# Optimization experiments

Hardware: AMD Instinct MI355X
Metric: run time of the kernel (lower is better)

The kernel has to match this reference:

```python
import jax, jax.numpy as jnp
import numpy as np

B, R, C, D = 4, 64, 64, 512   # batch, rows, cols, hidden_size
H, DH = 4, 128                # num_heads, channels per head
S = R * C                     # flattened attention length (raster order)
NEG = -1e6                    # mask value used by coltran


def setup_inputs():
    key = jax.random.key(0)
    ks = jax.random.split(key, 7)
    def w(k, shape, s=0.02):
        return jax.random.normal(k, shape, jnp.float32) * s
    return dict(
        x=jax.random.normal(ks[0], (B, R, C, D), jnp.float32),
        wq=w(ks[1], (D, H, DH)),
        wk=w(ks[2], (D, H, DH)),
        wv=w(ks[3], (D, H, DH)),
        wo=w(ks[4], (H, DH, D)),
        # relative_attention_bias_i: [num_heads, 2*length] per axis
        # (zero-init in the original; randomized here so the bias path is exercised)
        rel_row=w(ks[5], (H, 2 * R)),
        rel_col=w(ks[6], (H, 2 * C)),
    )


def _axis_bias(w, L):
    """att_utils.relative_attn_bias: [H, 2L] -> [H, Lq, Lk], b[h,q,k] = w[h, L-1 + k - q]."""
    pos = jnp.arange(L)
    idx = (L - 1) + pos[None, :] - pos[:, None]  # [Lq, Lk] in [0, 2L-2]
    return w[:, idx]


def reference(x, wq, wk, wv, wo, rel_row, rel_col):
    # q/k/v projections: contract channel axis into [H, DH]
    q = jnp.einsum('brcd,dhe->brche', x, wq) * (DH ** -0.5)
    k = jnp.einsum('brcd,dhe->brche', x, wk)
    v = jnp.einsum('brcd,dhe->brche', x, wv)
    q = q.reshape(B, S, H, DH)
    k = k.reshape(B, S, H, DH)
    v = v.reshape(B, S, H, DH)

    # factorized N-D relative attention bias -> [H, S, S]
    brow = _axis_bias(rel_row, R)  # [H, R, R]
    bcol = _axis_bias(rel_col, C)  # [H, C, C]
    bias = (brow[:, :, None, :, None] + bcol[:, None, :, None, :]).reshape(H, S, S)

    # 'future' mask in raster order: disallow k > q
    mask = jnp.triu(jnp.full((S, S), NEG, dtype=jnp.float32), 1)

    logits = jnp.einsum('bqhe,bkhe->bhqk', q, k) + bias[None] + mask[None, None]
    p = jax.nn.softmax(logits, axis=-1)
    o = jnp.einsum('bhqk,bkhe->bqhe', p, v)       # weighted sum over keys
    out = jnp.einsum('bqhe,hed->bqd', o, wo)      # final projection, contract_axes=2
    return out.reshape(B, R, C, D)
```

## Files before the change

### kernel.cpp

```cpp
#include <hip/hip_runtime.h>
#include <cstdint>

typedef unsigned short u16;
typedef __attribute__((ext_vector_type(8))) short short8;
typedef __attribute__((ext_vector_type(4))) short short4v;
typedef __attribute__((ext_vector_type(4))) float f32x4;
typedef __attribute__((ext_vector_type(4))) unsigned short u16x4;
typedef __attribute__((ext_vector_type(2))) float f32x2;
typedef __attribute__((ext_vector_type(2))) __bf16 bf16x2;


#if defined(__has_builtin)
#if __has_builtin(__builtin_amdgcn_mfma_f32_16x16x16bf16_1k)
#define HAVE_MFMA16 1
#endif
#endif

__device__ __forceinline__ uint32_t pk2(float a, float b) {
  f32x2 t;
  t[0] = a;
  t[1] = b;
  bf16x2 h = __builtin_convertvector(t, bf16x2);
  return __builtin_bit_cast(uint32_t, h);
}

__device__ __forceinline__ u16 f2b(float f) {
  return __builtin_bit_cast(u16, (__bf16)f);
}

__device__ __forceinline__ uint2 pkbf16x4(f32x4 v, float s) {
  uint2 r;
  r.x = pk2(v[0] * s, v[1] * s);
  r.y = pk2(v[2] * s, v[3] * s);
  return r;
}

__device__ __forceinline__ void dma16(const u16* g, u16* l) {
  __builtin_amdgcn_global_load_lds(
      (const __attribute__((address_space(1))) unsigned int*)(uintptr_t)g,
      (__attribute__((address_space(3))) unsigned int*)(uintptr_t)l, 16, 0, 0);
}

#define LDS_FENCE() asm volatile("s_waitcnt lgkmcnt(0)" ::: "memory")

__global__ __launch_bounds__(256) void xcast(const float* __restrict__ x,
                                             u16* __restrict__ xb) {
  const size_t i = (size_t)(blockIdx.x * 256 + threadIdx.x) * 8;
  const float4 a = *(const float4*)(x + i);
  const float4 b = *(const float4*)(x + i + 4);
  uint4 o;
  o.x = pk2(a.x, a.y);
  o.y = pk2(a.z, a.w);
  o.z = pk2(b.x, b.y);
  o.w = pk2(b.z, b.w);
  *(uint4*)(xb + i) = o;
}

__global__ __launch_bounds__(256) void transpose_all(const float* __restrict__ wq,
                                                     const float* __restrict__ wk,
                                                     const float* __restrict__ wv,
                                                     const float* __restrict__ wo,
                                                     u16* __restrict__ wT,
                                                     u16* __restrict__ woT) {
  __shared__ __align__(16) u16 T[64][68];
  const int mtx = blockIdx.y;
  const float* src = (mtx == 0) ? wq : (mtx == 1) ? wk : (mtx == 2) ? wv : wo;
  u16* dst = (mtx < 3) ? (wT + (size_t)mtx * 262144) : woT;
  const int tr = blockIdx.x >> 3, tc = blockIdx.x & 7;
  const int tid = threadIdx.x;
#pragma unroll
  for (int p = 0; p < 4; ++p) {
    int i = p * 256 + tid;
    int row = i >> 4, c4 = i & 15;
    float4 v = *(const float4*)(src + (size_t)(tr * 64 + row) * 512 + tc * 64 + c4 * 4);
    T[c4 * 4 + 0][row] = f2b(v.x);
    T[c4 * 4 + 1][row] = f2b(v.y);
    T[c4 * 4 + 2][row] = f2b(v.z);
    T[c4 * 4 + 3][row] = f2b(v.w);
  }
  __syncthreads();
#pragma unroll
  for (int p = 0; p < 4; ++p) {
    int i = p * 256 + tid;
    int row = i >> 4, c4 = i & 15;
    *(u16x4*)(dst + (size_t)(tc * 64 + row) * 512 + tr * 64 + c4 * 4) =
        *(const u16x4*)&T[row][c4 * 4];
  }
}

__global__ __launch_bounds__(512, 2) void qkv_gemm(const u16* __restrict__ xb,
                                                   const u16* __restrict__ wT_all,
                                                   u16* __restrict__ qbuf,
                                                   u16* __restrict__ kbuf,
                                                   u16* __restrict__ vtbuf) {
  __shared__ __align__(16) u16 smem[128 * 72 + 256 * 72];
  u16* As = smem;
  u16* Bs = smem + 128 * 72;
  const int tid = threadIdx.x;
  const int wave = tid >> 6, lane = tid & 63, quad = lane >> 4, l16 = lane & 15;
  const int wm = wave >> 2, wn = wave & 3;
  const int m0 = blockIdx.x * 128;
  const int which = blockIdx.y >> 1;
  const int n0 = (blockIdx.y & 1) * 256;
  const u16* wTb = wT_all + (size_t)which * 262144 + (size_t)n0 * 512;

  f32x4 acc[4][4];
  const f32x4 fz = {0.f, 0.f, 0.f, 0.f};
#pragma unroll
  for (int i = 0; i < 4; ++i)
#pragma unroll
    for (int j = 0; j < 4; ++j) acc[i][j] = fz;

  for (int k0 = 0; k0 < 512; k0 += 64) {
#pragma unroll
    for (int p = 0; p < 2; ++p) {
      int i = p * 512 + tid, row = i >> 3, c8 = i & 7;
      uint4 v = *(const uint4*)(xb + (size_t)(m0 + row) * 512 + k0 + c8 * 8);
      *(uint4*)&As[row * 72 + c8 * 8] = v;
    }
#pragma unroll
    for (int p = 0; p < 4; ++p) {
      int i = p * 512 + tid, row = i >> 3, c8 = i & 7;
      uint4 v = *(const uint4*)(wTb + (size_t)row * 512 + k0 + c8 * 8);
      *(uint4*)&Bs[row * 72 + c8 * 8] = v;
    }
    __syncthreads();
#pragma unroll
    for (int ks = 0; ks < 2; ++ks) {
      short8 xf[4], wf[4];
#pragma unroll
      for (int mt = 0; mt < 4; ++mt)
        xf[mt] = *(const short8*)&As[(wm * 64 + mt * 16 + l16) * 72 + ks * 32 + quad * 8];
#pragma unroll
      for (int nt = 0; nt < 4; ++nt)
        wf[nt] = *(const short8*)&Bs[(wn * 64 + nt * 16 + l16) * 72 + ks * 32 + quad * 8];
      if (which < 2) {
#pragma unroll
        for (int mt = 0; mt < 4; ++mt)
#pragma unroll
          for (int nt = 0; nt < 4; ++nt)
            acc[mt][nt] = __builtin_amdgcn_mfma_f32_16x16x32_bf16(wf[nt], xf[mt],
                                                                  acc[mt][nt], 0, 0, 0);
      } else {
#pragma unroll
        for (int mt = 0; mt < 4; ++mt)
#pragma unroll
          for (int nt = 0; nt < 4; ++nt)
            acc[mt][nt] = __builtin_amdgcn_mfma_f32_16x16x32_bf16(xf[mt], wf[nt],
                                                                  acc[mt][nt], 0, 0, 0);
      }
    }
    __syncthreads();
  }
  u16* sw = smem + wave * 3072;
  const int dhg0 = n0 + wn * 64;
  const int h = dhg0 >> 7, dhh0 = dhg0 & 127;
  const int bq = m0 >> 12;
  const int bh = bq * 4 + h;
  const int sl0 = (m0 & 4095) + wm * 64;

  if (which < 2) {
    const float scl = (which == 0) ? 0.08838834764831845f : 1.0f;
    u16* dst = (which == 0) ? qbuf : kbuf;
#pragma unroll
    for (int mt = 0; mt < 4; ++mt) {
      LDS_FENCE();
#pragma unroll
      for (int nt = 0; nt < 4; ++nt)
        *(uint2*)&sw[l16 * 68 + nt * 16 + quad * 4] = pkbf16x4(acc[mt][nt], scl);
      LDS_FENCE();
#pragma unroll
      for (int p = 0; p < 2; ++p) {
        const int sr = p * 8 + (lane >> 3), dl = (lane & 7) * 8;
        uint4 v = *(const uint4*)&sw[sr * 68 + dl];
        const int sl = sl0 + mt * 16 + sr;
        *(uint4*)(dst + ((size_t)(bh * 4096 + sl)) * 128 + dhh0 + dl) = v;
      }
    }
  } else {
#pragma unroll
    for (int p2 = 0; p2 < 2; ++p2) {
      LDS_FENCE();
#pragma unroll
      for (int m2 = 0; m2 < 2; ++m2) {
        const int mt = p2 * 2 + m2;
#pragma unroll
        for (int nt = 0; nt < 4; ++nt)
          *(uint2*)&sw[(nt * 16 + l16) * 36 + m2 * 16 + quad * 4] =
              pkbf16x4(acc[mt][nt], 1.0f);
      }
      LDS_FENCE();
#pragma unroll
      for (int j = 0; j < 4; ++j) {
        const int dl = j * 16 + (lane >> 2), so = (lane & 3) * 8;
        uint4 v = *(const uint4*)&sw[dl * 36 + so];
        const int sl = sl0 + p2 * 32 + so;
        *(uint4*)(vtbuf + ((size_t)(bh * 128 + dhh0 + dl)) * 4096 + sl) = v;
      }
    }
  }
}

__global__ __launch_bounds__(256, 4) void attn(const u16* __restrict__ qbuf,
                                               const u16* __restrict__ kbuf,
                                               const u16* __restrict__ vtbuf,
                                               const float* __restrict__ rel_row,
                                               const float* __restrict__ rel_col,
                                               u16* __restrict__ obuf) {
  __shared__ __align__(16) u16 KsF[64 * 128];
  __shared__ __align__(16) u16 VtF[128 * 64];
#ifndef HAVE_MFMA16
  __shared__ __align__(16) u16 Plds[4][16][72];
#endif
  __shared__ float rcol[128];
  __shared__ float rrow[128];

  const int tid = threadIdx.x;
  const int wave = tid >> 6, lane = tid & 63, quad = lane >> 4, l16 = lane & 15;
  const int g = blockIdx.x & 255, jq = blockIdx.x >> 8;
  const int t = g >> 4, bh = g & 15;
  const int qt = (jq == 0) ? (63 - t) : (jq == 1) ? t : (jq == 2) ? (47 - t) : (16 + t);
  const int b = bh >> 2, h = bh & 3;

  const float LOG2E = 1.4426950408889634f;
  if (tid < 128) rcol[tid] = rel_col[h * 128 + tid] * LOG2E;
  else rrow[tid - 128] = rel_row[h * 128 + (tid - 128)] * LOG2E;

  const int q_loc = wave * 16 + l16;
  const int q_glob = qt * 64 + q_loc;
  const int qc = q_loc;

  const u16* qrow = qbuf + ((size_t)bh * 4096 + q_glob) * 128;
  short8 qf[4];
#pragma unroll
  for (int ks = 0; ks < 4; ++ks) qf[ks] = *(const short8*)(qrow + ks * 32 + quad * 8);

  __syncthreads();

  float rc2[4][4];
#pragma unroll
  for (int nt = 0; nt < 4; ++nt)
#pragma unroll
    for (int r = 0; r < 4; ++r)
      rc2[nt][r] = rcol[63 + nt * 16 + quad * 4 + r - qc];

  const f32x4 fz = {0.f, 0.f, 0.f, 0.f};
  f32x4 oacc[8];
#pragma unroll
  for (int i = 0; i < 8; ++i) oacc[i] = fz;
  float l_run = 0.0f;

  const u16* kbase = kbuf + (size_t)bh * 4096 * 128;
  const u16* vbase = vtbuf + (size_t)bh * 128 * 4096;
  const int krow = tid >> 4, kcs = ((tid & 15) ^ (krow & 7)) * 8;
  const int vrow = tid >> 3, vcs = ((tid & 7) ^ (vrow & 7)) * 8;
  u16* kdst = KsF + wave * 512;
  u16* vdst = VtF + wave * 512;

  for (int kt = 0; kt <= qt; ++kt) {
    __syncthreads();
    {
      const u16* ksrc = kbase + (size_t)kt * 8192;
      const u16* vsrc = vbase + kt * 64;
#pragma unroll
      for (int j = 0; j < 4; ++j)
        dma16(ksrc + (size_t)(j * 16 + krow) * 128 + kcs, kdst + j * 2048);
#pragma unroll
      for (int j = 0; j < 4; ++j)
        dma16(vsrc + (size_t)(j * 32 + vrow) * 4096 + vcs, vdst + j * 2048);
    }
    __syncthreads();

    f32x4 sacc[4];
#pragma unroll
    for (int nt = 0; nt < 4; ++nt) sacc[nt] = fz;
    __builtin_amdgcn_s_setprio(1);
#pragma unroll
    for (int ks = 0; ks < 4; ++ks)
#pragma unroll
      for (int nt = 0; nt < 4; ++nt) {
        short8 kf = *(const short8*)&KsF[(nt * 16 + l16) * 128 +
                                         ((ks * 32 + quad * 8) ^ ((l16 & 7) * 8))];
        sacc[nt] = __builtin_amdgcn_mfma_f32_16x16x32_bf16(kf, qf[ks], sacc[nt], 0, 0, 0);
      }
    __builtin_amdgcn_s_setprio(0);

    const float browl = rrow[63 + kt - qt];
    const bool diag = (kt == qt);
    uint2 pd[4];
#pragma unroll
    for (int nt = 0; nt < 4; ++nt) {
      f32x4 pv;
#pragma unroll
      for (int r = 0; r < 4; ++r) {
        const int kc2 = nt * 16 + quad * 4 + r;
        float p = __builtin_amdgcn_exp2f(fmaf(sacc[nt][r], LOG2E, rc2[nt][r] + browl));
        if (diag && kc2 > qc) p = 0.0f;
        l_run += p;
        pv[r] = p;
      }
      pd[nt].x = pk2(pv[0], pv[1]);
      pd[nt].y = pk2(pv[2], pv[3]);
    }

#ifdef HAVE_MFMA16
    __builtin_amdgcn_s_setprio(1);
#pragma unroll
    for (int nt = 0; nt < 4; ++nt) {
      short4v pf = __builtin_bit_cast(short4v, pd[nt]);
#pragma unroll
      for (int mt = 0; mt < 8; ++mt) {
        short4v vf = *(const short4v*)&VtF[(mt * 16 + l16) * 64 +
                                           ((nt * 16 + quad * 4) ^ ((l16 & 7) * 8))];
        oacc[mt] = __builtin_amdgcn_mfma_f32_16x16x16bf16_1k(vf, pf, oacc[mt], 0, 0, 0);
      }
    }
    __builtin_amdgcn_s_setprio(0);
#else
#pragma unroll
    for (int nt = 0; nt < 4; ++nt)
      *(uint2*)&Plds[wave][l16][nt * 16 + quad * 4] = pd[nt];
#pragma unroll
    for (int ks2 = 0; ks2 < 2; ++ks2) {
      short8 pf = *(const short8*)&Plds[wave][l16][ks2 * 32 + quad * 8];
#pragma unroll
      for (int mt = 0; mt < 8; ++mt) {
        short8 vf = *(const short8*)&VtF[(mt * 16 + l16) * 64 +
                                         ((ks2 * 32 + quad * 8) ^ ((l16 & 7) * 8))];
        oacc[mt] = __builtin_amdgcn_mfma_f32_16x16x32_bf16(vf, pf, oacc[mt], 0, 0, 0);
      }
    }
#endif
  }

  l_run += __shfl_xor(l_run, 16);
  l_run += __shfl_xor(l_run, 32);
  const float inv_l = 1.0f / l_run;
  u16* orow = obuf + ((size_t)b * 4096 + q_glob) * 512 + h * 128;
#pragma unroll
  for (int mt = 0; mt < 8; ++mt)
    *(uint2*)(orow + mt * 16 + quad * 4) = pkbf16x4(oacc[mt], inv_l);
}

__global__ __launch_bounds__(512, 2) void out_gemm(const u16* __restrict__ obuf,
                                                   const u16* __restrict__ woT,
                                                   float* __restrict__ out) {
  __shared__ __align__(16) u16 smem[128 * 72 + 256 * 72];
  u16* As = smem;
  u16* Bs = smem + 128 * 72;
  const int tid = threadIdx.x;
  const int wave = tid >> 6, lane = tid & 63, quad = lane >> 4, l16 = lane & 15;
  const int wm = wave >> 2, wn = wave & 3;
  const int m0 = blockIdx.x * 128;
  const int n0 = blockIdx.y * 256;

  f32x4 acc[4][4];
  const f32x4 fz = {0.f, 0.f, 0.f, 0.f};
#pragma unroll
  for (int i = 0; i < 4; ++i)
#pragma unroll
    for (int j = 0; j < 4; ++j) acc[i][j] = fz;

  for (int k0 = 0; k0 < 512; k0 += 64) {
#pragma unroll
    for (int p = 0; p < 2; ++p) {
      int i = p * 512 + tid, row = i >> 3, c8 = i & 7;
      uint4 v = *(const uint4*)(obuf + (size_t)(m0 + row) * 512 + k0 + c8 * 8);
      *(uint4*)&As[row * 72 + c8 * 8] = v;
    }
#pragma unroll
    for (int p = 0; p < 4; ++p) {
      int i = p * 512 + tid, row = i >> 3, c8 = i & 7;
      uint4 v = *(const uint4*)(woT + (size_t)(n0 + row) * 512 + k0 + c8 * 8);
      *(uint4*)&Bs[row * 72 + c8 * 8] = v;
    }
    __syncthreads();
#pragma unroll
    for (int ks = 0; ks < 2; ++ks) {
      short8 of[4], wf[4];
#pragma unroll
      for (int mt = 0; mt < 4; ++mt)
        of[mt] = *(const short8*)&As[(wm * 64 + mt * 16 + l16) * 72 + ks * 32 + quad * 8];
#pragma unroll
      for (int nt = 0; nt < 4; ++nt)
        wf[nt] = *(const short8*)&Bs[(wn * 64 + nt * 16 + l16) * 72 + ks * 32 + quad * 8];
#pragma unroll
      for (int mt = 0; mt < 4; ++mt)
#pragma unroll
        for (int nt = 0; nt < 4; ++nt)
          acc[mt][nt] = __builtin_amdgcn_mfma_f32_16x16x32_bf16(wf[nt], of[mt],
                                                                acc[mt][nt], 0, 0, 0);
    }
    __syncthreads();
  }

  float* swf = (float*)smem + wave * 1536;
#pragma unroll
  for (int mt = 0; mt < 4; ++mt) {
    LDS_FENCE();
#pragma unroll
    for (int nt = 0; nt < 4; ++nt)
      *(f32x4*)&swf[l16 * 68 + nt * 16 + quad * 4] = acc[mt][nt];
    LDS_FENCE();
#pragma unroll
    for (int p = 0; p < 4; ++p) {
      const int sr = p * 4 + (lane >> 4), dl = l16 * 4;
      float4 v = *(const float4*)&swf[sr * 68 + dl];
      const int s = m0 + wm * 64 + mt * 16 + sr;
      *(float4*)(out + (size_t)s * 512 + n0 + wn * 64 + dl) = v;
    }
  }
}

extern "C" void kernel_launch(void* const* d_in, const int* in_sizes, int n_in,
                              void* d_out, int out_size, void* d_ws, size_t ws_size,
                              hipStream_t stream) {
  const float* x       = (const float*)d_in[0];
  const float* wq      = (const float*)d_in[1];
  const float* wk      = (const float*)d_in[2];
  const float* wv      = (const float*)d_in[3];
  const float* wo      = (const float*)d_in[4];
  const float* rel_row = (const float*)d_in[5];
  const float* rel_col = (const float*)d_in[6];
  float* out = (float*)d_out;

  char* ws = (char*)d_ws;
  u16* wT    = (u16*)(ws);
  u16* woT   = (u16*)(ws + 1572864);
  u16* qbuf  = (u16*)(ws + 2097152);
  u16* kbuf  = (u16*)(ws + 2097152 + 16777216);
  u16* vtbuf = (u16*)(ws + 2097152 + 2 * 16777216);
  u16* obuf  = (u16*)(ws + 2097152 + 3 * 16777216);
  u16* xb    = obuf;

  xcast<<<4096, 256, 0, stream>>>(x, xb);
  transpose_all<<<dim3(64, 4), 256, 0, stream>>>(wq, wk, wv, wo, wT, woT);
  qkv_gemm<<<dim3(128, 6), 512, 0, stream>>>(xb, wT, qbuf, kbuf, vtbuf);
  attn<<<1024, 256, 0, stream>>>(qbuf, kbuf, vtbuf, rel_row, rel_col, obuf);
  out_gemm<<<dim3(128, 2), 512, 0, stream>>>(obuf, woT, out);
}
```

Measured before the change: 298.6 us.

## Prefetch next K/V tile into registers instead of direct LDS DMA

Replaces global_load_lds DMA with register-staged loads of the next K/V tile, issued after the LDS write so global latency overlaps compute. It also switches the XOR-swizzled LDS layout to padded rows and simplifies block-to-tile mapping to descending qt order. The cost is extra VGPRs and LDS, which may lower occupancy, and the loss of the balanced causal-work interleave.

```diff
diff --git a/kernel.cpp b/kernel.cpp
--- a/kernel.cpp
+++ b/kernel.cpp
@@ -33,12 +33,6 @@
   r.x = pk2(v[0] * s, v[1] * s);
   r.y = pk2(v[2] * s, v[3] * s);
   return r;
-}
-
-__device__ __forceinline__ void dma16(const u16* g, u16* l) {
-  __builtin_amdgcn_global_load_lds(
-      (const __attribute__((address_space(1))) unsigned int*)(uintptr_t)g,
-      (__attribute__((address_space(3))) unsigned int*)(uintptr_t)l, 16, 0, 0);
 }
 
 #define LDS_FENCE() asm volatile("s_waitcnt lgkmcnt(0)" ::: "memory")
@@ -207,8 +201,8 @@
                                                const float* __restrict__ rel_row,
                                                const float* __restrict__ rel_col,
                                                u16* __restrict__ obuf) {
-  __shared__ __align__(16) u16 KsF[64 * 128];
-  __shared__ __align__(16) u16 VtF[128 * 64];
+  __shared__ __align__(16) u16 Ks[64][136];
+  __shared__ __align__(16) u16 Vt[128][72];
 #ifndef HAVE_MFMA16
   __shared__ __align__(16) u16 Plds[4][16][72];
 #endif
@@ -217,9 +211,8 @@
 
   const int tid = threadIdx.x;
   const int wave = tid >> 6, lane = tid & 63, quad = lane >> 4, l16 = lane & 15;
-  const int g = blockIdx.x & 255, jq = blockIdx.x >> 8;
-  const int t = g >> 4, bh = g & 15;
-  const int qt = (jq == 0) ? (63 - t) : (jq == 1) ? t : (jq == 2) ? (47 - t) : (16 + t);
+  const int bh = blockIdx.x & 15;
+  const int qt = 63 - (blockIdx.x >> 4);
   const int b = bh >> 2, h = bh & 3;
 
   const float LOG2E = 1.4426950408889634f;
@@ -252,24 +245,34 @@
 
   const u16* kbase = kbuf + (size_t)bh * 4096 * 128;
   const u16* vbase = vtbuf + (size_t)bh * 128 * 4096;
-  const int krow = tid >> 4, kcs = ((tid & 15) ^ (krow & 7)) * 8;
-  const int vrow = tid >> 3, vcs = ((tid & 7) ^ (vrow & 7)) * 8;
-  u16* kdst = KsF + wave * 512;
-  u16* vdst = VtF + wave * 512;
+  const int kr = tid >> 4, kc = (tid & 15) * 8;
+  const int vr = tid >> 3, vc = (tid & 7) * 8;
+
+  uint4 kreg[4], vreg[4];
+#pragma unroll
+  for (int j = 0; j < 4; ++j)
+    kreg[j] = *(const uint4*)(kbase + (size_t)(j * 16 + kr) * 128 + kc);
+#pragma unroll
+  for (int j = 0; j < 4; ++j)
+    vreg[j] = *(const uint4*)(vbase + (size_t)(j * 32 + vr) * 4096 + vc);
 
   for (int kt = 0; kt <= qt; ++kt) {
     __syncthreads();
-    {
-      const u16* ksrc = kbase + (size_t)kt * 8192;
-      const u16* vsrc = vbase + kt * 64;
+#pragma unroll
+    for (int j = 0; j < 4; ++j) *(uint4*)&Ks[j * 16 + kr][kc] = kreg[j];
+#pragma unroll
+    for (int j = 0; j < 4; ++j) *(uint4*)&Vt[j * 32 + vr][vc] = vreg[j];
+    __syncthreads();
+    if (kt < qt) {
+      const u16* ksrc = kbase + (size_t)(kt + 1) * 8192;
+      const u16* vsrc = vbase + (kt + 1) * 64;
 #pragma unroll
       for (int j = 0; j < 4; ++j)
-        dma16(ksrc + (size_t)(j * 16 + krow) * 128 + kcs, kdst + j * 2048);
+        kreg[j] = *(const uint4*)(ksrc + (size_t)(j * 16 + kr) * 128 + kc);
 #pragma unroll
       for (int j = 0; j < 4; ++j)
-        dma16(vsrc + (size_t)(j * 32 + vrow) * 4096 + vcs, vdst + j * 2048);
-    }
-    __syncthreads();
+        vreg[j] = *(const uint4*)(vsrc + (size_t)(j * 32 + vr) * 4096 + vc);
+    }
 
     f32x4 sacc[4];
 #pragma unroll
@@ -279,8 +282,7 @@
     for (int ks = 0; ks < 4; ++ks)
 #pragma unroll
       for (int nt = 0; nt < 4; ++nt) {
-        short8 kf = *(const short8*)&KsF[(nt * 16 + l16) * 128 +
-                                         ((ks * 32 + quad * 8) ^ ((l16 & 7) * 8))];
+        short8 kf = *(const short8*)&Ks[nt * 16 + l16][ks * 32 + quad * 8];
         sacc[nt] = __builtin_amdgcn_mfma_f32_16x16x32_bf16(kf, qf[ks], sacc[nt], 0, 0, 0);
       }
     __builtin_amdgcn_s_setprio(0);
@@ -310,8 +312,7 @@
       short4v pf = __builtin_bit_cast(short4v, pd[nt]);
 #pragma unroll
       for (int mt = 0; mt < 8; ++mt) {
-        short4v vf = *(const short4v*)&VtF[(mt * 16 + l16) * 64 +
-                                           ((nt * 16 + quad * 4) ^ ((l16 & 7) * 8))];
+        short4v vf = *(const short4v*)&Vt[mt * 16 + l16][nt * 16 + quad * 4];
         oacc[mt] = __builtin_amdgcn_mfma_f32_16x16x16bf16_1k(vf, pf, oacc[mt], 0, 0, 0);
       }
     }
@@ -325,8 +326,7 @@
       short8 pf = *(const short8*)&Plds[wave][l16][ks2 * 32 + quad * 8];
 #pragma unroll
       for (int mt = 0; mt < 8; ++mt) {
-        short8 vf = *(const short8*)&VtF[(mt * 16 + l16) * 64 +
-                                         ((ks2 * 32 + quad * 8) ^ ((l16 & 7) * 8))];
+        short8 vf = *(const short8*)&Vt[mt * 16 + l16][ks2 * 32 + quad * 8];
         oacc[mt] = __builtin_amdgcn_mfma_f32_16x16x32_bf16(vf, pf, oacc[mt], 0, 0, 0);
       }
     }
```

Measured after the change: 508.9 us. 1.7x slower.

## Balance causal attention work by pairing rows and splitting long rows across blocks

Applied to the files above, without the earlier changes.

The causal attention grid changes from one query tile per block to balanced work units. Each half-0 block handles one short row plus the first half of a long row, and each half-1 block handles the second half of that long row. The partial outputs and softmax denominators go to fp32 workspace, and a new onorm kernel combines and normalizes them. This gives every block the same number of key tiles, removing tail imbalance, at the cost of extra fp32 partial traffic and an additional kernel launch.

```diff
diff --git a/kernel.cpp b/kernel.cpp
--- a/kernel.cpp
+++ b/kernel.cpp
@@ -206,7 +206,9 @@
                                                const u16* __restrict__ vtbuf,
                                                const float* __restrict__ rel_row,
                                                const float* __restrict__ rel_col,
-                                               u16* __restrict__ obuf) {
+                                               u16* __restrict__ obuf,
+                                               float* __restrict__ opart,
+                                               float* __restrict__ lpart) {
   __shared__ __align__(16) u16 KsF[64 * 128];
   __shared__ __align__(16) u16 VtF[128 * 64];
 #ifndef HAVE_MFMA16
@@ -217,9 +219,8 @@
 
   const int tid = threadIdx.x;
   const int wave = tid >> 6, lane = tid & 63, quad = lane >> 4, l16 = lane & 15;
-  const int g = blockIdx.x & 255, jq = blockIdx.x >> 8;
-  const int t = g >> 4, bh = g & 15;
-  const int qt = (jq == 0) ? (63 - t) : (jq == 1) ? t : (jq == 2) ? (47 - t) : (16 + t);
+  const int jid = blockIdx.x;
+  const int bh = jid & 15, p = (jid >> 4) & 31, half = jid >> 9;
   const int b = bh >> 2, h = bh & 3;
 
   const float LOG2E = 1.4426950408889634f;
@@ -227,13 +228,7 @@
   else rrow[tid - 128] = rel_row[h * 128 + (tid - 128)] * LOG2E;
 
   const int q_loc = wave * 16 + l16;
-  const int q_glob = qt * 64 + q_loc;
   const int qc = q_loc;
-
-  const u16* qrow = qbuf + ((size_t)bh * 4096 + q_glob) * 128;
-  short8 qf[4];
-#pragma unroll
-  for (int ks = 0; ks < 4; ++ks) qf[ks] = *(const short8*)(qrow + ks * 32 + quad * 8);
 
   __syncthreads();
 
@@ -245,11 +240,6 @@
       rc2[nt][r] = rcol[63 + nt * 16 + quad * 4 + r - qc];
 
   const f32x4 fz = {0.f, 0.f, 0.f, 0.f};
-  f32x4 oacc[8];
-#pragma unroll
-  for (int i = 0; i < 8; ++i) oacc[i] = fz;
-  float l_run = 0.0f;
-
   const u16* kbase = kbuf + (size_t)bh * 4096 * 128;
   const u16* vbase = vtbuf + (size_t)bh * 128 * 4096;
   const int krow = tid >> 4, kcs = ((tid & 15) ^ (krow & 7)) * 8;
@@ -257,89 +247,141 @@
   u16* kdst = KsF + wave * 512;
   u16* vdst = VtF + wave * 512;
 
-  for (int kt = 0; kt <= qt; ++kt) {
-    __syncthreads();
-    {
-      const u16* ksrc = kbase + (size_t)kt * 8192;
-      const u16* vsrc = vbase + kt * 64;
-#pragma unroll
-      for (int j = 0; j < 4; ++j)
-        dma16(ksrc + (size_t)(j * 16 + krow) * 128 + kcs, kdst + j * 2048);
-#pragma unroll
-      for (int j = 0; j < 4; ++j)
-        dma16(vsrc + (size_t)(j * 32 + vrow) * 4096 + vcs, vdst + j * 2048);
-    }
-    __syncthreads();
-
-    f32x4 sacc[4];
-#pragma unroll
-    for (int nt = 0; nt < 4; ++nt) sacc[nt] = fz;
-    __builtin_amdgcn_s_setprio(1);
-#pragma unroll
-    for (int ks = 0; ks < 4; ++ks)
+  auto run_row = [&](int r, int ktb, int kte, bool direct) {
+    const u16* qrow = qbuf + ((size_t)bh * 4096 + r * 64 + q_loc) * 128;
+    short8 qf[4];
+#pragma unroll
+    for (int ks = 0; ks < 4; ++ks) qf[ks] = *(const short8*)(qrow + ks * 32 + quad * 8);
+    f32x4 oacc[8];
+#pragma unroll
+    for (int i = 0; i < 8; ++i) oacc[i] = fz;
+    float l_run = 0.0f;
+
+    for (int kt = ktb; kt < kte; ++kt) {
+      __syncthreads();
+      {
+        const u16* ksrc = kbase + (size_t)kt * 8192;
+        const u16* vsrc = vbase + kt * 64;
+#pragma unroll
+        for (int j = 0; j < 4; ++j)
+          dma16(ksrc + (size_t)(j * 16 + krow) * 128 + kcs, kdst + j * 2048);
+#pragma unroll
+        for (int j = 0; j < 4; ++j)
+          dma16(vsrc + (size_t)(j * 32 + vrow) * 4096 + vcs, vdst + j * 2048);
+      }
+      __syncthreads();
+
+      f32x4 sacc[4];
+#pragma unroll
+      for (int nt = 0; nt < 4; ++nt) sacc[nt] = fz;
+      __builtin_amdgcn_s_setprio(1);
+#pragma unroll
+      for (int ks = 0; ks < 4; ++ks)
+#pragma unroll
+        for (int nt = 0; nt < 4; ++nt) {
+          short8 kf = *(const short8*)&KsF[(nt * 16 + l16) * 128 +
+                                           ((ks * 32 + quad * 8) ^ ((l16 & 7) * 8))];
+          sacc[nt] = __builtin_amdgcn_mfma_f32_16x16x32_bf16(kf, qf[ks], sacc[nt], 0, 0, 0);
+        }
+      __builtin_amdgcn_s_setprio(0);
+
+      const float browl = rrow[63 + kt - r];
+      const bool diag = (kt == r);
+      uint2 pd[4];
 #pragma unroll
       for (int nt = 0; nt < 4; ++nt) {
-        short8 kf = *(const short8*)&KsF[(nt * 16 + l16) * 128 +
-                                         ((ks * 32 + quad * 8) ^ ((l16 & 7) * 8))];
-        sacc[nt] = __builtin_amdgcn_mfma_f32_16x16x32_bf16(kf, qf[ks], sacc[nt], 0, 0, 0);
-      }
-    __builtin_amdgcn_s_setprio(0);
-
-    const float browl = rrow[63 + kt - qt];
-    const bool diag = (kt == qt);
-    uint2 pd[4];
-#pragma unroll
-    for (int nt = 0; nt < 4; ++nt) {
-      f32x4 pv;
-#pragma unroll
-      for (int r = 0; r < 4; ++r) {
-        const int kc2 = nt * 16 + quad * 4 + r;
-        float p = __builtin_amdgcn_exp2f(fmaf(sacc[nt][r], LOG2E, rc2[nt][r] + browl));
-        if (diag && kc2 > qc) p = 0.0f;
-        l_run += p;
-        pv[r] = p;
-      }
-      pd[nt].x = pk2(pv[0], pv[1]);
-      pd[nt].y = pk2(pv[2], pv[3]);
-    }
+        f32x4 pv;
+#pragma unroll
+        for (int rr = 0; rr < 4; ++rr) {
+          const int kc2 = nt * 16 + quad * 4 + rr;
+          float pe = __builtin_amdgcn_exp2f(fmaf(sacc[nt][rr], LOG2E, rc2[nt][rr] + browl));
+          if (diag && kc2 > qc) pe = 0.0f;
+          l_run += pe;
+          pv[rr] = pe;
+        }
+        pd[nt].x = pk2(pv[0], pv[1]);
+        pd[nt].y = pk2(pv[2], pv[3]);
+      }
 
 #ifdef HAVE_MFMA16
-    __builtin_amdgcn_s_setprio(1);
-#pragma unroll
-    for (int nt = 0; nt < 4; ++nt) {
-      short4v pf = __builtin_bit_cast(short4v, pd[nt]);
-#pragma unroll
-      for (int mt = 0; mt < 8; ++mt) {
-        short4v vf = *(const short4v*)&VtF[(mt * 16 + l16) * 64 +
-                                           ((nt * 16 + quad * 4) ^ ((l16 & 7) * 8))];
-        oacc[mt] = __builtin_amdgcn_mfma_f32_16x16x16bf16_1k(vf, pf, oacc[mt], 0, 0, 0);
-      }
-    }
-    __builtin_amdgcn_s_setprio(0);
+      __builtin_amdgcn_s_setprio(1);
+#pragma unroll
+      for (int nt = 0; nt < 4; ++nt) {
+        short4v pf = __builtin_bit_cast(short4v, pd[nt]);
+#pragma unroll
+        for (int mt = 0; mt < 8; ++mt) {
+          short4v vf = *(const short4v*)&VtF[(mt * 16 + l16) * 64 +
+                                             ((nt * 16 + quad * 4) ^ ((l16 & 7) * 8))];
+          oacc[mt] = __builtin_amdgcn_mfma_f32_16x16x16bf16_1k(vf, pf, oacc[mt], 0, 0, 0);
+        }
+      }
+      __builtin_amdgcn_s_setprio(0);
 #else
 #pragma unroll
-    for (int nt = 0; nt < 4; ++nt)
-      *(uint2*)&Plds[wave][l16][nt * 16 + quad * 4] = pd[nt];
-#pragma unroll
-    for (int ks2 = 0; ks2 < 2; ++ks2) {
-      short8 pf = *(const short8*)&Plds[wave][l16][ks2 * 32 + quad * 8];
-#pragma unroll
-      for (int mt = 0; mt < 8; ++mt) {
-        short8 vf = *(const short8*)&VtF[(mt * 16 + l16) * 64 +
-                                         ((ks2 * 32 + quad * 8) ^ ((l16 & 7) * 8))];
-        oacc[mt] = __builtin_amdgcn_mfma_f32_16x16x32_bf16(vf, pf, oacc[mt], 0, 0, 0);
-      }
-    }
+      for (int nt = 0; nt < 4; ++nt)
+        *(uint2*)&Plds[wave][l16][nt * 16 + quad * 4] = pd[nt];
+#pragma unroll
+      for (int ks2 = 0; ks2 < 2; ++ks2) {
+        short8 pf = *(const short8*)&Plds[wave][l16][ks2 * 32 + quad * 8];
+#pragma unroll
+        for (int mt = 0; mt < 8; ++mt) {
+          short8 vf = *(const short8*)&VtF[(mt * 16 + l16) * 64 +
+                                           ((ks2 * 32 + quad * 8) ^ ((l16 & 7) * 8))];
+          oacc[mt] = __builtin_amdgcn_mfma_f32_16x16x32_bf16(vf, pf, oacc[mt], 0, 0, 0);
+        }
+      }
 #endif
-  }
-
-  l_run += __shfl_xor(l_run, 16);
-  l_run += __shfl_xor(l_run, 32);
-  const float inv_l = 1.0f / l_run;
-  u16* orow = obuf + ((size_t)b * 4096 + q_glob) * 512 + h * 128;
-#pragma unroll
-  for (int mt = 0; mt < 8; ++mt)
-    *(uint2*)(orow + mt * 16 + quad * 4) = pkbf16x4(oacc[mt], inv_l);
+    }
+
+    l_run += __shfl_xor(l_run, 16);
+    l_run += __shfl_xor(l_run, 32);
+    if (direct) {
+      const float inv_l = 1.0f / l_run;
+      u16* orow = obuf + ((size_t)b * 4096 + r * 64 + q_loc) * 512 + h * 128;
+#pragma unroll
+      for (int mt = 0; mt < 8; ++mt)
+        *(uint2*)(orow + mt * 16 + quad * 4) = pkbf16x4(oacc[mt], inv_l);
+    } else {
+      const size_t qi = (size_t)((half * 16 + bh) * 32 + (r - 32)) * 64 + q_loc;
+      float* od = opart + qi * 128;
+#pragma unroll
+      for (int mt = 0; mt < 8; ++mt)
+        *(f32x4*)(od + mt * 16 + quad * 4) = oacc[mt];
+      if (quad == 0) lpart[qi] = l_run;
+    }
+  };
+
+  if (half == 0) {
+    run_row(p, 0, p + 1, true);
+    run_row(63 - p, 0, 32 - p, false);
+  } else {
+    run_row(63 - p, 32 - p, 64 - p, false);
+  }
+}
+
+__global__ __launch_bounds__(256) void onorm(const float* __restrict__ opart,
+                                             const float* __restrict__ lpart,
+                                             u16* __restrict__ obuf) {
+  const int gi = blockIdx.x * 256 + threadIdx.x;
+  const int d8 = (gi & 15) * 8;
+  const int qi = gi >> 4;
+  const int q = qi & 63, rr = (qi >> 6) & 31, bh = qi >> 11;
+  const float inv = 1.0f / (lpart[qi] + lpart[32768 + qi]);
+  const float* s0 = opart + (size_t)qi * 128 + d8;
+  const float* s1 = s0 + 4194304;
+  f32x4 a0 = *(const f32x4*)s0;
+  f32x4 b0 = *(const f32x4*)(s0 + 4);
+  f32x4 a1 = *(const f32x4*)s1;
+  f32x4 b1 = *(const f32x4*)(s1 + 4);
+  f32x4 sa = a0 + a1, sb = b0 + b1;
+  uint4 o;
+  o.x = pk2(sa[0] * inv, sa[1] * inv);
+  o.y = pk2(sa[2] * inv, sa[3] * inv);
+  o.z = pk2(sb[0] * inv, sb[1] * inv);
+  o.w = pk2(sb[2] * inv, sb[3] * inv);
+  const int b = bh >> 2, h = bh & 3;
+  const int q_glob = (32 + rr) * 64 + q;
+  *(uint4*)(obuf + ((size_t)b * 4096 + q_glob) * 512 + h * 128 + d8) = o;
 }
 
 __global__ __launch_bounds__(512, 2) void out_gemm(const u16* __restrict__ obuf,
@@ -431,11 +473,14 @@
   u16* kbuf  = (u16*)(ws + 2097152 + 16777216);
   u16* vtbuf = (u16*)(ws + 2097152 + 2 * 16777216);
   u16* obuf  = (u16*)(ws + 2097152 + 3 * 16777216);
+  float* opart = (float*)(ws + 2097152 + 4 * 16777216);
+  float* lpart = (float*)(ws + 2097152 + 6 * 16777216);
   u16* xb    = obuf;
 
   xcast<<<4096, 256, 0, stream>>>(x, xb);
   transpose_all<<<dim3(64, 4), 256, 0, stream>>>(wq, wk, wv, wo, wT, woT);
   qkv_gemm<<<dim3(128, 6), 512, 0, stream>>>(xb, wT, qbuf, kbuf, vtbuf);
-  attn<<<1024, 256, 0, stream>>>(qbuf, kbuf, vtbuf, rel_row, rel_col, obuf);
+  attn<<<1024, 256, 0, stream>>>(qbuf, kbuf, vtbuf, rel_row, rel_col, obuf, opart, lpart);
+  onorm<<<2048, 256, 0, stream>>>(opart, lpart, obuf);
   out_gemm<<<dim3(128, 2), 512, 0, stream>>>(obuf, woT, out);
 }
```

Measured after the change: 277.6 us. -7.0%, faster.
